# Kernel tuning notes

Hardware: AMD Instinct MI355X
Metric: run time of the kernel (lower is better)

Reference implementation:

```python
import jax, jax.numpy as jnp
import numpy as np

N_NODES = 50000
N_EDGES = 800000
IN_FEATS, HIDDEN_FEATS, NUM_CLASSES = 64, 64, 32


def setup_inputs() -> dict:
    key = jax.random.key(0)
    ks = jax.random.split(key, 9)
    features = jax.random.normal(ks[0], (N_NODES, IN_FEATS), dtype=jnp.float32)
    src = jax.random.randint(ks[1], (N_EDGES,), 0, N_NODES, dtype=jnp.int32)
    dst = jax.random.randint(ks[2], (N_EDGES,), 0, N_NODES, dtype=jnp.int32)
    def lin(k, fan_in, fan_out):
        bound = 1.0 / np.sqrt(fan_in)
        return jax.random.uniform(k, (fan_in, fan_out), jnp.float32, -bound, bound)
    W_self1 = lin(ks[3], IN_FEATS, HIDDEN_FEATS)
    W_neigh1 = lin(ks[4], IN_FEATS, HIDDEN_FEATS)
    b1 = jnp.zeros((HIDDEN_FEATS,), jnp.float32)
    W_self2 = lin(ks[5], HIDDEN_FEATS, NUM_CLASSES)
    W_neigh2 = lin(ks[6], HIDDEN_FEATS, NUM_CLASSES)
    b2 = jnp.zeros((NUM_CLASSES,), jnp.float32)
    return {"features": features, "W_self1": W_self1, "W_neigh1": W_neigh1, "b1": b1,
            "W_self2": W_self2, "W_neigh2": W_neigh2, "b2": b2, "src": src, "dst": dst}


def _sage_mean(x, W_self, W_neigh, b, src, dst, n_nodes):
    # mean over in-neighbors: edge (u, v) sends x[u] into v
    agg = jax.ops.segment_sum(x[src], dst, num_segments=n_nodes)          # [N, F]
    deg = jax.ops.segment_sum(jnp.ones((src.shape[0],), x.dtype), dst,
                              num_segments=n_nodes)                        # [N]
    h_neigh = agg / jnp.maximum(deg, 1.0)[:, None]                         # zero-in-degree -> 0
    return x @ W_self + h_neigh @ W_neigh + b


def reference(features, W_self1, W_neigh1, b1, W_self2, W_neigh2, b2, src, dst):
    n = features.shape[0]
    h = jax.nn.relu(_sage_mean(features, W_self1, W_neigh1, b1, src, dst, n))
    return _sage_mean(h, W_self2, W_neigh2, b2, src, dst, n)
```

## Files before the change

### kernel.cpp

```cpp
#include <hip/hip_runtime.h>

#define N_NODES 50000
#define N_EDGES 800000
#define NB 196
#define PBLOCKS 128
#define CHUNK 6250
#define SCAN_N (NB * PBLOCKS)
#define GEMM_BLOCKS 782

typedef unsigned short ushort_t;
typedef __attribute__((ext_vector_type(8))) short bf16x8;
typedef __attribute__((ext_vector_type(4))) float f32x4;

__device__ __forceinline__ float bflo(unsigned int u) {
    return __uint_as_float(u << 16);
}
__device__ __forceinline__ float bfhi(unsigned int u) {
    return __uint_as_float(u & 0xffff0000u);
}
__device__ __forceinline__ ushort_t f2bf(float f) {
    unsigned int x = __float_as_uint(f);
    return (ushort_t)((x + 0x7fffu + ((x >> 16) & 1u)) >> 16);
}
__device__ __forceinline__ unsigned int pack_bf(float lo, float hi) {
    return (unsigned int)f2bf(lo) | ((unsigned int)f2bf(hi) << 16);
}
__device__ __forceinline__ void split_bf(float v, short& hi, short& lo) {
    ushort_t h = f2bf(v);
    float r = v - __uint_as_float((unsigned int)h << 16);
    hi = (short)h;
    lo = (short)f2bf(r);
}


__global__ __launch_bounds__(1024)
void part_scan(const int* __restrict__ blocktot, int* __restrict__ blockstart) {
    __shared__ int psum[1024];
    constexpr int PER = (SCAN_N + 1023) / 1024;
    const int t = threadIdx.x;
    const int base = t * PER;
    int local[PER];
    int s = 0;
#pragma unroll
    for (int i = 0; i < PER; ++i) {
        int idx = base + i;
        int v = (idx < SCAN_N) ? blocktot[idx] : 0;
        local[i] = s;
        s += v;
    }
    psum[t] = s;
    __syncthreads();
    for (int off = 1; off < 1024; off <<= 1) {
        int add = (t >= off) ? psum[t - off] : 0;
        __syncthreads();
        psum[t] += add;
        __syncthreads();
    }
    const int tbase = psum[t] - s;
#pragma unroll
    for (int i = 0; i < PER; ++i) {
        int idx = base + i;
        if (idx < SCAN_N) blockstart[idx] = tbase + local[i];
    }
    if (t == 1023) blockstart[SCAN_N] = psum[1023];
}

__global__ __launch_bounds__(256)
void part_write(const int* __restrict__ src, const int* __restrict__ dst,
                const int* __restrict__ blockstart, unsigned int* __restrict__ brec) {
    __shared__ int cur[NB];
    for (int i = threadIdx.x; i < NB; i += 256)
        cur[i] = blockstart[i * PBLOCKS + blockIdx.x];
    __syncthreads();
    const int e0 = blockIdx.x * CHUNK;
    const int e1 = e0 + CHUNK;
    for (int e = e0 + (int)threadIdx.x; e < e1; e += 256) {
        int d = dst[e];
        int s = src[e];
        int pos = atomicAdd(&cur[d >> 8], 1);
        brec[pos] = ((unsigned int)(d & 255) << 16) | (unsigned int)s;
    }
}

__global__ __launch_bounds__(256)
void bucket_fill(const int* __restrict__ blockstart,
                 const unsigned int* __restrict__ brec,
                 int* __restrict__ csr_src, int* __restrict__ row_ptr) {
    __shared__ int cnt[256];
    __shared__ int cur[256];
    const int b = blockIdx.x;
    const int node0 = b * 256;
    const int w0 = blockstart[b * PBLOCKS];
    const int w1 = blockstart[(b + 1) * PBLOCKS];
    const int t = threadIdx.x;
    cnt[t] = 0;
    __syncthreads();
    for (int i = w0 + t; i < w1; i += 256)
        atomicAdd(&cnt[brec[i] >> 16], 1);
    __syncthreads();
    const int v = cnt[t];
    cur[t] = v;
    __syncthreads();
    for (int off = 1; off < 256; off <<= 1) {
        int add = (t >= off) ? cur[t - off] : 0;
        __syncthreads();
        cur[t] += add;
        __syncthreads();
    }
    const int excl = cur[t] - v;
    const int node = node0 + t;
    if (node <= N_NODES) row_ptr[node] = w0 + excl;
    __syncthreads();
    cur[t] = w0 + excl;
    __syncthreads();
    for (int i = w0 + t; i < w1; i += 256) {
        unsigned int r = brec[i];
        int pos = atomicAdd(&cur[r >> 16], 1);
        csr_src[pos] = (int)(r & 0xffffu);
    }
}

__global__ __launch_bounds__(256)
void gemm128_and_count(const float* __restrict__ A,
                       const float* __restrict__ B1,
                       const float* __restrict__ B2,
                       ushort_t* __restrict__ Cself,
                       ushort_t* __restrict__ Cn,
                       const int* __restrict__ dst,
                       int* __restrict__ blocktot) {
    __shared__ int hist[NB];

    if (blockIdx.x >= GEMM_BLOCKS) {
        const int pb = blockIdx.x - GEMM_BLOCKS;
        for (int i = threadIdx.x; i < NB; i += 256) hist[i] = 0;
        __syncthreads();
        const int e0 = pb * CHUNK;
        const int e1 = e0 + CHUNK;
        for (int e = e0 + (int)threadIdx.x; e < e1; e += 256)
            atomicAdd(&hist[dst[e] >> 8], 1);
        __syncthreads();
        for (int i = threadIdx.x; i < NB; i += 256)
            blocktot[i * PBLOCKS + pb] = hist[i];
        return;
    }

    const int l  = threadIdx.x & 63;
    const int w  = threadIdx.x >> 6;
    const int lr = l & 15;
    const int lk = (l >> 4) << 3;

    bf16x8 bhi[2][2], blo[2][2];
#pragma unroll
    for (int nt = 0; nt < 2; ++nt) {
        const int n = w * 32 + nt * 16 + lr;
        const float* Bp = (n < 64) ? (B1 + n) : (B2 + (n - 64));
#pragma unroll
        for (int ks = 0; ks < 2; ++ks) {
#pragma unroll
            for (int j = 0; j < 8; ++j) {
                float bv = Bp[(size_t)(ks * 32 + lk + j) * 64];
                short h, lo;
                split_bf(bv, h, lo);
                bhi[nt][ks][j] = h;
                blo[nt][ks][j] = lo;
            }
        }
    }

    const int m0 = blockIdx.x * 64;
    f32x4 acc[4][2];
#pragma unroll
    for (int mt = 0; mt < 4; ++mt)
#pragma unroll
        for (int nt = 0; nt < 2; ++nt) {
            f32x4 z = {0.f, 0.f, 0.f, 0.f};
            acc[mt][nt] = z;
        }

#pragma unroll
    for (int mt = 0; mt < 4; ++mt) {
        const int m = m0 + mt * 16 + lr;
        const bool valid = (m < N_NODES);
        const float* Ap = A + (size_t)m * 64 + lk;
#pragma unroll
        for (int ks = 0; ks < 2; ++ks) {
            float4 f0, f1;
            if (valid) {
                f0 = *(const float4*)(Ap + ks * 32);
                f1 = *(const float4*)(Ap + ks * 32 + 4);
            } else {
                f0 = make_float4(0.f, 0.f, 0.f, 0.f);
                f1 = f0;
            }
            const float fv[8] = {f0.x, f0.y, f0.z, f0.w, f1.x, f1.y, f1.z, f1.w};
            bf16x8 ahi, alo;
#pragma unroll
            for (int j = 0; j < 8; ++j) {
                short h, lo;
                split_bf(fv[j], h, lo);
                ahi[j] = h;
                alo[j] = lo;
            }
#pragma unroll
            for (int nt = 0; nt < 2; ++nt) {
                acc[mt][nt] = __builtin_amdgcn_mfma_f32_16x16x32_bf16(
                    ahi, bhi[nt][ks], acc[mt][nt], 0, 0, 0);
                acc[mt][nt] = __builtin_amdgcn_mfma_f32_16x16x32_bf16(
                    alo, bhi[nt][ks], acc[mt][nt], 0, 0, 0);
                acc[mt][nt] = __builtin_amdgcn_mfma_f32_16x16x32_bf16(
                    ahi, blo[nt][ks], acc[mt][nt], 0, 0, 0);
            }
        }
    }

#pragma unroll
    for (int mt = 0; mt < 4; ++mt) {
        const int mbase = m0 + mt * 16 + ((l >> 4) << 2);
#pragma unroll
        for (int nt = 0; nt < 2; ++nt) {
            const int n = w * 32 + nt * 16 + lr;
            ushort_t* T = (n < 64) ? (Cself + n) : (Cn + (n - 64));
#pragma unroll
            for (int r = 0; r < 4; ++r) {
                const int m = mbase + r;
                if (m < N_NODES) T[(size_t)m * 64] = f2bf(acc[mt][nt][r]);
            }
        }
    }
}

__global__ __launch_bounds__(256)
void gemm_cat64_bf16(const ushort_t* __restrict__ A,
                     const float* __restrict__ B1,
                     const float* __restrict__ B2,
                     ushort_t* __restrict__ Cself,
                     ushort_t* __restrict__ Cn) {
    const int l  = threadIdx.x & 63;
    const int w  = threadIdx.x >> 6;
    const int lr = l & 15;
    const int lk = (l >> 4) << 3;

    const int n = w * 16 + lr;
    const float* Bp = (n < 32) ? (B1 + n) : (B2 + (n - 32));
    bf16x8 bhi[2], blo[2];
#pragma unroll
    for (int ks = 0; ks < 2; ++ks) {
#pragma unroll
        for (int j = 0; j < 8; ++j) {
            float bv = Bp[(size_t)(ks * 32 + lk + j) * 32];
            short h, lo;
            split_bf(bv, h, lo);
            bhi[ks][j] = h;
            blo[ks][j] = lo;
        }
    }

    const int m0 = blockIdx.x * 64;
    f32x4 acc[4];
#pragma unroll
    for (int mt = 0; mt < 4; ++mt) {
        f32x4 z = {0.f, 0.f, 0.f, 0.f};
        acc[mt] = z;
    }

#pragma unroll
    for (int mt = 0; mt < 4; ++mt) {
        const int m = m0 + mt * 16 + lr;
        const bool valid = (m < N_NODES);
#pragma unroll
        for (int ks = 0; ks < 2; ++ks) {
            bf16x8 a;
            if (valid) {
                a = *(const bf16x8*)&A[(size_t)m * 64 + ks * 32 + lk];
            } else {
                bf16x8 z = {0, 0, 0, 0, 0, 0, 0, 0};
                a = z;
            }
            acc[mt] = __builtin_amdgcn_mfma_f32_16x16x32_bf16(a, bhi[ks], acc[mt], 0, 0, 0);
            acc[mt] = __builtin_amdgcn_mfma_f32_16x16x32_bf16(a, blo[ks], acc[mt], 0, 0, 0);
        }
    }

    ushort_t* T = (n < 32) ? (Cself + n) : (Cn + (n - 32));
#pragma unroll
    for (int mt = 0; mt < 4; ++mt) {
        const int mbase = m0 + mt * 16 + ((l >> 4) << 2);
#pragma unroll
        for (int r = 0; r < 4; ++r) {
            const int m = mbase + r;
            if (m < N_NODES) T[(size_t)m * 32] = f2bf(acc[mt][r]);
        }
    }
}

template <int F, bool RELU, bool OBF16>
__global__ __launch_bounds__(256)
void gather_epilogue(const ushort_t* __restrict__ Tself,
                     const ushort_t* __restrict__ Tn,
                     const int* __restrict__ row_ptr,
                     const int* __restrict__ csr_src, const float* __restrict__ bias,
                     void* __restrict__ outv) {
    constexpr int LPR = F / 8;
    constexpr int R   = 64 / LPR;
    int v = (blockIdx.x * blockDim.x + threadIdx.x) >> 6;
    int lane = threadIdx.x & 63;
    int r = lane / LPR;
    int c = lane % LPR;
    if (v >= N_NODES) return;
    int start = row_ptr[v];
    int cnt   = row_ptr[v + 1] - start;

    float a[8];
#pragma unroll
    for (int i = 0; i < 8; ++i) a[i] = 0.f;

#define ACC8(u)                                           \
    a[0] += bflo(u.x); a[1] += bfhi(u.x);                 \
    a[2] += bflo(u.y); a[3] += bfhi(u.y);                 \
    a[4] += bflo(u.z); a[5] += bfhi(u.z);                 \
    a[6] += bflo(u.w); a[7] += bfhi(u.w);

    int t = r;
    for (; t + 3 * R < cnt; t += 4 * R) {
        int s0 = csr_src[start + t];
        int s1 = csr_src[start + t + R];
        int s2 = csr_src[start + t + 2 * R];
        int s3 = csr_src[start + t + 3 * R];
        uint4 u0 = *(const uint4*)&Tn[(size_t)s0 * F + c * 8];
        uint4 u1 = *(const uint4*)&Tn[(size_t)s1 * F + c * 8];
        uint4 u2 = *(const uint4*)&Tn[(size_t)s2 * F + c * 8];
        uint4 u3 = *(const uint4*)&Tn[(size_t)s3 * F + c * 8];
        ACC8(u0) ACC8(u1) ACC8(u2) ACC8(u3)
    }
    if (t + R < cnt) {
        int s0 = csr_src[start + t];
        int s1 = csr_src[start + t + R];
        uint4 u0 = *(const uint4*)&Tn[(size_t)s0 * F + c * 8];
        uint4 u1 = *(const uint4*)&Tn[(size_t)s1 * F + c * 8];
        ACC8(u0) ACC8(u1)
        t += 2 * R;
    }
    if (t < cnt) {
        int s = csr_src[start + t];
        uint4 u = *(const uint4*)&Tn[(size_t)s * F + c * 8];
        ACC8(u)
    }
#undef ACC8

#pragma unroll
    for (int off = LPR; off < 64; off <<= 1) {
#pragma unroll
        for (int i = 0; i < 8; ++i) a[i] += __shfl_xor(a[i], off);
    }

    if (r == 0) {
        const float inv = 1.0f / (float)max(cnt, 1);
        uint4 su = *(const uint4*)&Tself[(size_t)v * F + c * 8];
        float4 bA = *(const float4*)&bias[c * 8];
        float4 bB = *(const float4*)&bias[c * 8 + 4];
        float o[8];
        o[0] = bflo(su.x) + a[0] * inv + bA.x;
        o[1] = bfhi(su.x) + a[1] * inv + bA.y;
        o[2] = bflo(su.y) + a[2] * inv + bA.z;
        o[3] = bfhi(su.y) + a[3] * inv + bA.w;
        o[4] = bflo(su.z) + a[4] * inv + bB.x;
        o[5] = bfhi(su.z) + a[5] * inv + bB.y;
        o[6] = bflo(su.w) + a[6] * inv + bB.z;
        o[7] = bfhi(su.w) + a[7] * inv + bB.w;
        if (RELU) {
#pragma unroll
            for (int i = 0; i < 8; ++i) o[i] = fmaxf(o[i], 0.f);
        }
        if (OBF16) {
            ushort_t* out = (ushort_t*)outv;
            uint4 p;
            p.x = pack_bf(o[0], o[1]); p.y = pack_bf(o[2], o[3]);
            p.z = pack_bf(o[4], o[5]); p.w = pack_bf(o[6], o[7]);
            *(uint4*)&out[(size_t)v * F + c * 8] = p;
        } else {
            float* out = (float*)outv;
            *(float4*)&out[(size_t)v * F + c * 8]     = make_float4(o[0], o[1], o[2], o[3]);
            *(float4*)&out[(size_t)v * F + c * 8 + 4] = make_float4(o[4], o[5], o[6], o[7]);
        }
    }
}

extern "C" void kernel_launch(void* const* d_in, const int* in_sizes, int n_in,
                              void* d_out, int out_size, void* d_ws, size_t ws_size,
                              hipStream_t stream) {
    const float* features = (const float*)d_in[0];
    const float* W_self1  = (const float*)d_in[1];
    const float* W_neigh1 = (const float*)d_in[2];
    const float* b1       = (const float*)d_in[3];
    const float* W_self2  = (const float*)d_in[4];
    const float* W_neigh2 = (const float*)d_in[5];
    const float* b2       = (const float*)d_in[6];
    const int*   src      = (const int*)d_in[7];
    const int*   dst      = (const int*)d_in[8];

    ushort_t* Tself1 = (ushort_t*)d_ws;
    ushort_t* Tn1    = Tself1 + (size_t)N_NODES * 64;
    ushort_t* h      = Tn1 + (size_t)N_NODES * 64;
    int* row_ptr     = (int*)(h + (size_t)N_NODES * 64);
    int* csr_src     = row_ptr + (N_NODES + 1);
    unsigned int* brec = (unsigned int*)(csr_src + N_EDGES);
    int* blocktot    = (int*)(brec + N_EDGES);
    int* blockstart  = blocktot + SCAN_N;

    ushort_t* Tself2 = Tself1;
    ushort_t* Tn2    = Tself1 + (size_t)N_NODES * 32;

    const int gather_blocks = (N_NODES + 3) / 4;

    gemm128_and_count<<<GEMM_BLOCKS + PBLOCKS, 256, 0, stream>>>(
        features, W_self1, W_neigh1, Tself1, Tn1, dst, blocktot);
    part_scan<<<1, 1024, 0, stream>>>(blocktot, blockstart);
    part_write<<<PBLOCKS, 256, 0, stream>>>(src, dst, blockstart, brec);
    bucket_fill<<<NB, 256, 0, stream>>>(blockstart, brec, csr_src, row_ptr);

    gather_epilogue<64, true, true><<<gather_blocks, 256, 0, stream>>>(
        Tself1, Tn1, row_ptr, csr_src, b1, h);

    gemm_cat64_bf16<<<GEMM_BLOCKS, 256, 0, stream>>>(h, W_self2, W_neigh2, Tself2, Tn2);

    gather_epilogue<32, false, false><<<gather_blocks, 256, 0, stream>>>(
        Tself2, Tn2, row_ptr, csr_src, b2, d_out);
}
```

Measured before the change: 185.9 us.

## Fuse layer-2 GEMM into layer-1 gather and fold partition scan into consumers

Drops the separate single-block scan kernel. part_write and bucket_fill now each recompute their partition offsets directly from the per-block histograms, and the number of partition blocks doubles. The layer-1 gather epilogue now also does the 64x64 second-layer projection per node, using register-held weight columns and wavefront shuffles. This removes the hidden-activation round trip and one GEMM launch. In exchange it adds redundant scan work in every block, 64 live weight registers per thread, and a scalar FMA projection in place of MFMA.

```diff
diff --git a/kernel.cpp b/kernel.cpp
--- a/kernel.cpp
+++ b/kernel.cpp
@@ -3,9 +3,8 @@
 #define N_NODES 50000
 #define N_EDGES 800000
 #define NB 196
-#define PBLOCKS 128
-#define CHUNK 6250
-#define SCAN_N (NB * PBLOCKS)
+#define PBLOCKS 256
+#define CHUNK 3125
 #define GEMM_BLOCKS 782
 
 typedef unsigned short ushort_t;
@@ -30,94 +29,6 @@
     float r = v - __uint_as_float((unsigned int)h << 16);
     hi = (short)h;
     lo = (short)f2bf(r);
-}
-
-
-__global__ __launch_bounds__(1024)
-void part_scan(const int* __restrict__ blocktot, int* __restrict__ blockstart) {
-    __shared__ int psum[1024];
-    constexpr int PER = (SCAN_N + 1023) / 1024;
-    const int t = threadIdx.x;
-    const int base = t * PER;
-    int local[PER];
-    int s = 0;
-#pragma unroll
-    for (int i = 0; i < PER; ++i) {
-        int idx = base + i;
-        int v = (idx < SCAN_N) ? blocktot[idx] : 0;
-        local[i] = s;
-        s += v;
-    }
-    psum[t] = s;
-    __syncthreads();
-    for (int off = 1; off < 1024; off <<= 1) {
-        int add = (t >= off) ? psum[t - off] : 0;
-        __syncthreads();
-        psum[t] += add;
-        __syncthreads();
-    }
-    const int tbase = psum[t] - s;
-#pragma unroll
-    for (int i = 0; i < PER; ++i) {
-        int idx = base + i;
-        if (idx < SCAN_N) blockstart[idx] = tbase + local[i];
-    }
-    if (t == 1023) blockstart[SCAN_N] = psum[1023];
-}
-
-__global__ __launch_bounds__(256)
-void part_write(const int* __restrict__ src, const int* __restrict__ dst,
-                const int* __restrict__ blockstart, unsigned int* __restrict__ brec) {
-    __shared__ int cur[NB];
-    for (int i = threadIdx.x; i < NB; i += 256)
-        cur[i] = blockstart[i * PBLOCKS + blockIdx.x];
-    __syncthreads();
-    const int e0 = blockIdx.x * CHUNK;
-    const int e1 = e0 + CHUNK;
-    for (int e = e0 + (int)threadIdx.x; e < e1; e += 256) {
-        int d = dst[e];
-        int s = src[e];
-        int pos = atomicAdd(&cur[d >> 8], 1);
-        brec[pos] = ((unsigned int)(d & 255) << 16) | (unsigned int)s;
-    }
-}
-
-__global__ __launch_bounds__(256)
-void bucket_fill(const int* __restrict__ blockstart,
-                 const unsigned int* __restrict__ brec,
-                 int* __restrict__ csr_src, int* __restrict__ row_ptr) {
-    __shared__ int cnt[256];
-    __shared__ int cur[256];
-    const int b = blockIdx.x;
-    const int node0 = b * 256;
-    const int w0 = blockstart[b * PBLOCKS];
-    const int w1 = blockstart[(b + 1) * PBLOCKS];
-    const int t = threadIdx.x;
-    cnt[t] = 0;
-    __syncthreads();
-    for (int i = w0 + t; i < w1; i += 256)
-        atomicAdd(&cnt[brec[i] >> 16], 1);
-    __syncthreads();
-    const int v = cnt[t];
-    cur[t] = v;
-    __syncthreads();
-    for (int off = 1; off < 256; off <<= 1) {
-        int add = (t >= off) ? cur[t - off] : 0;
-        __syncthreads();
-        cur[t] += add;
-        __syncthreads();
-    }
-    const int excl = cur[t] - v;
-    const int node = node0 + t;
-    if (node <= N_NODES) row_ptr[node] = w0 + excl;
-    __syncthreads();
-    cur[t] = w0 + excl;
-    __syncthreads();
-    for (int i = w0 + t; i < w1; i += 256) {
-        unsigned int r = brec[i];
-        int pos = atomicAdd(&cur[r >> 16], 1);
-        csr_src[pos] = (int)(r & 0xffffu);
-    }
 }
 
 __global__ __launch_bounds__(256)
@@ -230,67 +141,194 @@
 }
 
 __global__ __launch_bounds__(256)
-void gemm_cat64_bf16(const ushort_t* __restrict__ A,
-                     const float* __restrict__ B1,
-                     const float* __restrict__ B2,
-                     ushort_t* __restrict__ Cself,
-                     ushort_t* __restrict__ Cn) {
-    const int l  = threadIdx.x & 63;
-    const int w  = threadIdx.x >> 6;
-    const int lr = l & 15;
-    const int lk = (l >> 4) << 3;
-
-    const int n = w * 16 + lr;
-    const float* Bp = (n < 32) ? (B1 + n) : (B2 + (n - 32));
-    bf16x8 bhi[2], blo[2];
-#pragma unroll
-    for (int ks = 0; ks < 2; ++ks) {
-#pragma unroll
-        for (int j = 0; j < 8; ++j) {
-            float bv = Bp[(size_t)(ks * 32 + lk + j) * 32];
-            short h, lo;
-            split_bf(bv, h, lo);
-            bhi[ks][j] = h;
-            blo[ks][j] = lo;
-        }
-    }
-
-    const int m0 = blockIdx.x * 64;
-    f32x4 acc[4];
-#pragma unroll
-    for (int mt = 0; mt < 4; ++mt) {
-        f32x4 z = {0.f, 0.f, 0.f, 0.f};
-        acc[mt] = z;
-    }
-
-#pragma unroll
-    for (int mt = 0; mt < 4; ++mt) {
-        const int m = m0 + mt * 16 + lr;
-        const bool valid = (m < N_NODES);
-#pragma unroll
-        for (int ks = 0; ks < 2; ++ks) {
-            bf16x8 a;
-            if (valid) {
-                a = *(const bf16x8*)&A[(size_t)m * 64 + ks * 32 + lk];
-            } else {
-                bf16x8 z = {0, 0, 0, 0, 0, 0, 0, 0};
-                a = z;
-            }
-            acc[mt] = __builtin_amdgcn_mfma_f32_16x16x32_bf16(a, bhi[ks], acc[mt], 0, 0, 0);
-            acc[mt] = __builtin_amdgcn_mfma_f32_16x16x32_bf16(a, blo[ks], acc[mt], 0, 0, 0);
-        }
-    }
-
-    ushort_t* T = (n < 32) ? (Cself + n) : (Cn + (n - 32));
-#pragma unroll
-    for (int mt = 0; mt < 4; ++mt) {
-        const int mbase = m0 + mt * 16 + ((l >> 4) << 2);
-#pragma unroll
-        for (int r = 0; r < 4; ++r) {
-            const int m = mbase + r;
-            if (m < N_NODES) T[(size_t)m * 32] = f2bf(acc[mt][r]);
-        }
-    }
+void part_write(const int* __restrict__ src, const int* __restrict__ dst,
+                const int* __restrict__ blocktot, unsigned int* __restrict__ brec) {
+    __shared__ int ssum[256];
+    __shared__ int cur[NB];
+    const int pb = blockIdx.x;
+    const int t  = threadIdx.x;
+
+    int rsum = 0, mypart = 0;
+    if (t < NB) {
+        const int* rp = blocktot + t * PBLOCKS;
+#pragma unroll 8
+        for (int j = 0; j < PBLOCKS; ++j) {
+            if (j == pb) mypart = rsum;
+            rsum += rp[j];
+        }
+    }
+    ssum[t] = (t < NB) ? rsum : 0;
+    __syncthreads();
+    for (int off = 1; off < 256; off <<= 1) {
+        int add = (t >= off) ? ssum[t - off] : 0;
+        __syncthreads();
+        ssum[t] += add;
+        __syncthreads();
+    }
+    if (t < NB) cur[t] = (ssum[t] - rsum) + mypart;
+    __syncthreads();
+
+    const int e0 = pb * CHUNK;
+    const int e1 = e0 + CHUNK;
+    for (int e = e0 + t; e < e1; e += 256) {
+        int d = dst[e];
+        int s = src[e];
+        int pos = atomicAdd(&cur[d >> 8], 1);
+        brec[pos] = ((unsigned int)(d & 255) << 16) | (unsigned int)s;
+    }
+}
+
+__global__ __launch_bounds__(256)
+void bucket_fill(const int* __restrict__ blocktot,
+                 const unsigned int* __restrict__ brec,
+                 int* __restrict__ csr_src, int* __restrict__ row_ptr) {
+    __shared__ int ssum[256];
+    __shared__ int cnt[256];
+    __shared__ int cur[256];
+    const int b = blockIdx.x;
+    const int node0 = b * 256;
+    const int t = threadIdx.x;
+
+    int rsum = 0;
+    if (t < NB) {
+        const int* rp = blocktot + t * PBLOCKS;
+#pragma unroll 8
+        for (int j = 0; j < PBLOCKS; ++j) rsum += rp[j];
+    }
+    ssum[t] = (t < NB) ? rsum : 0;
+    __syncthreads();
+    for (int off = 1; off < 256; off <<= 1) {
+        int add = (t >= off) ? ssum[t - off] : 0;
+        __syncthreads();
+        ssum[t] += add;
+        __syncthreads();
+    }
+    const int w0 = (b == 0) ? 0 : ssum[b - 1];
+    const int w1 = ssum[b];
+    __syncthreads();
+
+    cnt[t] = 0;
+    __syncthreads();
+    for (int i = w0 + t; i < w1; i += 256)
+        atomicAdd(&cnt[brec[i] >> 16], 1);
+    __syncthreads();
+    const int v = cnt[t];
+    cur[t] = v;
+    __syncthreads();
+    for (int off = 1; off < 256; off <<= 1) {
+        int add = (t >= off) ? cur[t - off] : 0;
+        __syncthreads();
+        cur[t] += add;
+        __syncthreads();
+    }
+    const int excl = cur[t] - v;
+    const int node = node0 + t;
+    if (node <= N_NODES) row_ptr[node] = w0 + excl;
+    __syncthreads();
+    cur[t] = w0 + excl;
+    __syncthreads();
+    for (int i = w0 + t; i < w1; i += 256) {
+        unsigned int r = brec[i];
+        int pos = atomicAdd(&cur[r >> 16], 1);
+        csr_src[pos] = (int)(r & 0xffffu);
+    }
+}
+
+__global__ __launch_bounds__(256)
+void gather1_fused(const ushort_t* __restrict__ Tself,
+                   const ushort_t* __restrict__ Tn,
+                   const int* __restrict__ row_ptr,
+                   const int* __restrict__ csr_src,
+                   const float* __restrict__ bias,
+                   const float* __restrict__ Ws2,
+                   const float* __restrict__ Wn2,
+                   ushort_t* __restrict__ Tself2,
+                   ushort_t* __restrict__ Tn2) {
+    constexpr int F = 64;
+    constexpr int LPR = 8;
+    constexpr int R = 8;
+    const int lane = threadIdx.x & 63;
+
+    float wcol[64];
+    {
+        const float* Wp = (lane < 32) ? (Ws2 + lane) : (Wn2 + (lane - 32));
+#pragma unroll
+        for (int k = 0; k < 64; ++k) wcol[k] = Wp[(size_t)k * 32];
+    }
+
+    int v = (blockIdx.x * blockDim.x + threadIdx.x) >> 6;
+    if (v >= N_NODES) return;
+    const int r = lane / LPR;
+    const int c = lane % LPR;
+    int start = row_ptr[v];
+    int cnt   = row_ptr[v + 1] - start;
+
+    float a[8];
+#pragma unroll
+    for (int i = 0; i < 8; ++i) a[i] = 0.f;
+
+#define ACC8(u)                                           \
+    a[0] += bflo(u.x); a[1] += bfhi(u.x);                 \
+    a[2] += bflo(u.y); a[3] += bfhi(u.y);                 \
+    a[4] += bflo(u.z); a[5] += bfhi(u.z);                 \
+    a[6] += bflo(u.w); a[7] += bfhi(u.w);
+
+    int t = r;
+    for (; t + 3 * R < cnt; t += 4 * R) {
+        int s0 = csr_src[start + t];
+        int s1 = csr_src[start + t + R];
+        int s2 = csr_src[start + t + 2 * R];
+        int s3 = csr_src[start + t + 3 * R];
+        uint4 u0 = *(const uint4*)&Tn[(size_t)s0 * F + c * 8];
+        uint4 u1 = *(const uint4*)&Tn[(size_t)s1 * F + c * 8];
+        uint4 u2 = *(const uint4*)&Tn[(size_t)s2 * F + c * 8];
+        uint4 u3 = *(const uint4*)&Tn[(size_t)s3 * F + c * 8];
+        ACC8(u0) ACC8(u1) ACC8(u2) ACC8(u3)
+    }
+    if (t + R < cnt) {
+        int s0 = csr_src[start + t];
+        int s1 = csr_src[start + t + R];
+        uint4 u0 = *(const uint4*)&Tn[(size_t)s0 * F + c * 8];
+        uint4 u1 = *(const uint4*)&Tn[(size_t)s1 * F + c * 8];
+        ACC8(u0) ACC8(u1)
+        t += 2 * R;
+    }
+    if (t < cnt) {
+        int s = csr_src[start + t];
+        uint4 u = *(const uint4*)&Tn[(size_t)s * F + c * 8];
+        ACC8(u)
+    }
+#undef ACC8
+
+#pragma unroll
+    for (int off = LPR; off < 64; off <<= 1) {
+#pragma unroll
+        for (int i = 0; i < 8; ++i) a[i] += __shfl_xor(a[i], off);
+    }
+
+    const float inv = 1.0f / (float)max(cnt, 1);
+    uint4 su = *(const uint4*)&Tself[(size_t)v * F + c * 8];
+    float4 bA = *(const float4*)&bias[c * 8];
+    float4 bB = *(const float4*)&bias[c * 8 + 4];
+    float o[8];
+    o[0] = bflo(su.x) + a[0] * inv + bA.x;
+    o[1] = bfhi(su.x) + a[1] * inv + bA.y;
+    o[2] = bflo(su.y) + a[2] * inv + bA.z;
+    o[3] = bfhi(su.y) + a[3] * inv + bA.w;
+    o[4] = bflo(su.z) + a[4] * inv + bB.x;
+    o[5] = bfhi(su.z) + a[5] * inv + bB.y;
+    o[6] = bflo(su.w) + a[6] * inv + bB.z;
+    o[7] = bfhi(su.w) + a[7] * inv + bB.w;
+#pragma unroll
+    for (int i = 0; i < 8; ++i) o[i] = fmaxf(o[i], 0.f);
+
+    float o2 = 0.f;
+#pragma unroll
+    for (int k = 0; k < 64; ++k)
+        o2 = fmaf(__shfl(o[k & 7], k >> 3), wcol[k], o2);
+
+    if (lane < 32) Tself2[(size_t)v * 32 + lane] = f2bf(o2);
+    else           Tn2[(size_t)v * 32 + (lane - 32)] = f2bf(o2);
 }
 
 template <int F, bool RELU, bool OBF16>
@@ -400,29 +438,23 @@
 
     ushort_t* Tself1 = (ushort_t*)d_ws;
     ushort_t* Tn1    = Tself1 + (size_t)N_NODES * 64;
-    ushort_t* h      = Tn1 + (size_t)N_NODES * 64;
-    int* row_ptr     = (int*)(h + (size_t)N_NODES * 64);
+    ushort_t* T2     = Tn1 + (size_t)N_NODES * 64;
+    int* row_ptr     = (int*)(T2 + (size_t)N_NODES * 64);
     int* csr_src     = row_ptr + (N_NODES + 1);
     unsigned int* brec = (unsigned int*)(csr_src + N_EDGES);
     int* blocktot    = (int*)(brec + N_EDGES);
-    int* blockstart  = blocktot + SCAN_N;
-
-    ushort_t* Tself2 = Tself1;
-    ushort_t* Tn2    = Tself1 + (size_t)N_NODES * 32;
+
+    ushort_t* Tself2 = T2;
+    ushort_t* Tn2    = T2 + (size_t)N_NODES * 32;
 
     const int gather_blocks = (N_NODES + 3) / 4;
 
     gemm128_and_count<<<GEMM_BLOCKS + PBLOCKS, 256, 0, stream>>>(
         features, W_self1, W_neigh1, Tself1, Tn1, dst, blocktot);
-    part_scan<<<1, 1024, 0, stream>>>(blocktot, blockstart);
-    part_write<<<PBLOCKS, 256, 0, stream>>>(src, dst, blockstart, brec);
-    bucket_fill<<<NB, 256, 0, stream>>>(blockstart, brec, csr_src, row_ptr);
-
-    gather_epilogue<64, true, true><<<gather_blocks, 256, 0, stream>>>(
-        Tself1, Tn1, row_ptr, csr_src, b1, h);
-
-    gemm_cat64_bf16<<<GEMM_BLOCKS, 256, 0, stream>>>(h, W_self2, W_neigh2, Tself2, Tn2);
-
+    part_write<<<PBLOCKS, 256, 0, stream>>>(src, dst, blocktot, brec);
+    bucket_fill<<<NB, 256, 0, stream>>>(blocktot, brec, csr_src, row_ptr);
+    gather1_fused<<<gather_blocks, 256, 0, stream>>>(
+        Tself1, Tn1, row_ptr, csr_src, b1, W_self2, W_neigh2, Tself2, Tn2);
     gather_epilogue<32, false, false><<<gather_blocks, 256, 0, stream>>>(
         Tself2, Tn2, row_ptr, csr_src, b2, d_out);
 }
```

New measurement: 200.3 us. +7.8%, slower.

## Fold partition scan into write/fill kernels and gather two nodes per wave

Applied to the files above, without the earlier changes.

Removes the single-block part_scan launch. Each part_write and bucket_fill block now recomputes the bucket offsets redundantly from blocktot using row sums and a shared-memory scan. The partition block count doubles and the chunk halves. The gather kernel now handles two nodes per 64-lane wave, reading up to 32 neighbor indices cooperatively and broadcasting them with shuffles so all neighbor loads are issued at once, with a loop for the tail. This trades a serial launch and index-load latency for redundant scan work in every block and a shorter reduction.

```diff
diff --git a/kernel.cpp b/kernel.cpp
--- a/kernel.cpp
+++ b/kernel.cpp
@@ -3,9 +3,8 @@
 #define N_NODES 50000
 #define N_EDGES 800000
 #define NB 196
-#define PBLOCKS 128
-#define CHUNK 6250
-#define SCAN_N (NB * PBLOCKS)
+#define PBLOCKS 256
+#define CHUNK 3125
 #define GEMM_BLOCKS 782
 
 typedef unsigned short ushort_t;
@@ -30,94 +29,6 @@
     float r = v - __uint_as_float((unsigned int)h << 16);
     hi = (short)h;
     lo = (short)f2bf(r);
-}
-
-
-__global__ __launch_bounds__(1024)
-void part_scan(const int* __restrict__ blocktot, int* __restrict__ blockstart) {
-    __shared__ int psum[1024];
-    constexpr int PER = (SCAN_N + 1023) / 1024;
-    const int t = threadIdx.x;
-    const int base = t * PER;
-    int local[PER];
-    int s = 0;
-#pragma unroll
-    for (int i = 0; i < PER; ++i) {
-        int idx = base + i;
-        int v = (idx < SCAN_N) ? blocktot[idx] : 0;
-        local[i] = s;
-        s += v;
-    }
-    psum[t] = s;
-    __syncthreads();
-    for (int off = 1; off < 1024; off <<= 1) {
-        int add = (t >= off) ? psum[t - off] : 0;
-        __syncthreads();
-        psum[t] += add;
-        __syncthreads();
-    }
-    const int tbase = psum[t] - s;
-#pragma unroll
-    for (int i = 0; i < PER; ++i) {
-        int idx = base + i;
-        if (idx < SCAN_N) blockstart[idx] = tbase + local[i];
-    }
-    if (t == 1023) blockstart[SCAN_N] = psum[1023];
-}
-
-__global__ __launch_bounds__(256)
-void part_write(const int* __restrict__ src, const int* __restrict__ dst,
-                const int* __restrict__ blockstart, unsigned int* __restrict__ brec) {
-    __shared__ int cur[NB];
-    for (int i = threadIdx.x; i < NB; i += 256)
-        cur[i] = blockstart[i * PBLOCKS + blockIdx.x];
-    __syncthreads();
-    const int e0 = blockIdx.x * CHUNK;
-    const int e1 = e0 + CHUNK;
-    for (int e = e0 + (int)threadIdx.x; e < e1; e += 256) {
-        int d = dst[e];
-        int s = src[e];
-        int pos = atomicAdd(&cur[d >> 8], 1);
-        brec[pos] = ((unsigned int)(d & 255) << 16) | (unsigned int)s;
-    }
-}
-
-__global__ __launch_bounds__(256)
-void bucket_fill(const int* __restrict__ blockstart,
-                 const unsigned int* __restrict__ brec,
-                 int* __restrict__ csr_src, int* __restrict__ row_ptr) {
-    __shared__ int cnt[256];
-    __shared__ int cur[256];
-    const int b = blockIdx.x;
-    const int node0 = b * 256;
-    const int w0 = blockstart[b * PBLOCKS];
-    const int w1 = blockstart[(b + 1) * PBLOCKS];
-    const int t = threadIdx.x;
-    cnt[t] = 0;
-    __syncthreads();
-    for (int i = w0 + t; i < w1; i += 256)
-        atomicAdd(&cnt[brec[i] >> 16], 1);
-    __syncthreads();
-    const int v = cnt[t];
-    cur[t] = v;
-    __syncthreads();
-    for (int off = 1; off < 256; off <<= 1) {
-        int add = (t >= off) ? cur[t - off] : 0;
-        __syncthreads();
-        cur[t] += add;
-        __syncthreads();
-    }
-    const int excl = cur[t] - v;
-    const int node = node0 + t;
-    if (node <= N_NODES) row_ptr[node] = w0 + excl;
-    __syncthreads();
-    cur[t] = w0 + excl;
-    __syncthreads();
-    for (int i = w0 + t; i < w1; i += 256) {
-        unsigned int r = brec[i];
-        int pos = atomicAdd(&cur[r >> 16], 1);
-        csr_src[pos] = (int)(r & 0xffffu);
-    }
 }
 
 __global__ __launch_bounds__(256)
@@ -226,6 +137,100 @@
                 if (m < N_NODES) T[(size_t)m * 64] = f2bf(acc[mt][nt][r]);
             }
         }
+    }
+}
+
+__global__ __launch_bounds__(256)
+void part_write(const int* __restrict__ src, const int* __restrict__ dst,
+                const int* __restrict__ blocktot, unsigned int* __restrict__ brec) {
+    __shared__ int ssum[256];
+    __shared__ int cur[NB];
+    const int pb = blockIdx.x;
+    const int t  = threadIdx.x;
+
+    int rsum = 0, mypart = 0;
+    if (t < NB) {
+        const int* rp = blocktot + t * PBLOCKS;
+#pragma unroll 8
+        for (int j = 0; j < PBLOCKS; ++j) {
+            if (j == pb) mypart = rsum;
+            rsum += rp[j];
+        }
+    }
+    ssum[t] = (t < NB) ? rsum : 0;
+    __syncthreads();
+    for (int off = 1; off < 256; off <<= 1) {
+        int add = (t >= off) ? ssum[t - off] : 0;
+        __syncthreads();
+        ssum[t] += add;
+        __syncthreads();
+    }
+    if (t < NB) cur[t] = (ssum[t] - rsum) + mypart;
+    __syncthreads();
+
+    const int e0 = pb * CHUNK;
+    const int e1 = e0 + CHUNK;
+    for (int e = e0 + t; e < e1; e += 256) {
+        int d = dst[e];
+        int s = src[e];
+        int pos = atomicAdd(&cur[d >> 8], 1);
+        brec[pos] = ((unsigned int)(d & 255) << 16) | (unsigned int)s;
+    }
+}
+
+__global__ __launch_bounds__(256)
+void bucket_fill(const int* __restrict__ blocktot,
+                 const unsigned int* __restrict__ brec,
+                 int* __restrict__ csr_src, int* __restrict__ row_ptr) {
+    __shared__ int ssum[256];
+    __shared__ int cnt[256];
+    __shared__ int cur[256];
+    const int b = blockIdx.x;
+    const int node0 = b * 256;
+    const int t = threadIdx.x;
+
+    int rsum = 0;
+    if (t < NB) {
+        const int* rp = blocktot + t * PBLOCKS;
+#pragma unroll 8
+        for (int j = 0; j < PBLOCKS; ++j) rsum += rp[j];
+    }
+    ssum[t] = (t < NB) ? rsum : 0;
+    __syncthreads();
+    for (int off = 1; off < 256; off <<= 1) {
+        int add = (t >= off) ? ssum[t - off] : 0;
+        __syncthreads();
+        ssum[t] += add;
+        __syncthreads();
+    }
+    const int w0 = (b == 0) ? 0 : ssum[b - 1];
+    const int w1 = ssum[b];
+    __syncthreads();
+
+    cnt[t] = 0;
+    __syncthreads();
+    for (int i = w0 + t; i < w1; i += 256)
+        atomicAdd(&cnt[brec[i] >> 16], 1);
+    __syncthreads();
+    const int v = cnt[t];
+    cur[t] = v;
+    __syncthreads();
+    for (int off = 1; off < 256; off <<= 1) {
+        int add = (t >= off) ? cur[t - off] : 0;
+        __syncthreads();
+        cur[t] += add;
+        __syncthreads();
+    }
+    const int excl = cur[t] - v;
+    const int node = node0 + t;
+    if (node <= N_NODES) row_ptr[node] = w0 + excl;
+    __syncthreads();
+    cur[t] = w0 + excl;
+    __syncthreads();
+    for (int i = w0 + t; i < w1; i += 256) {
+        unsigned int r = brec[i];
+        int pos = atomicAdd(&cur[r >> 16], 1);
+        csr_src[pos] = (int)(r & 0xffffu);
     }
 }
 
@@ -300,15 +305,18 @@
                      const int* __restrict__ row_ptr,
                      const int* __restrict__ csr_src, const float* __restrict__ bias,
                      void* __restrict__ outv) {
-    constexpr int LPR = F / 8;
-    constexpr int R   = 64 / LPR;
-    int v = (blockIdx.x * blockDim.x + threadIdx.x) >> 6;
-    int lane = threadIdx.x & 63;
-    int r = lane / LPR;
-    int c = lane % LPR;
+    constexpr int LPR  = F / 8;
+    constexpr int G    = 32 / LPR;
+    constexpr int MAXJ = 32 / G;
+    const int lane = threadIdx.x & 63;
+    const int half = lane >> 5;
+    const int hl   = lane & 31;
+    const int r = hl / LPR;
+    const int c = hl % LPR;
+    const int v = (((int)blockIdx.x * (int)blockDim.x + (int)threadIdx.x) >> 6) * 2 + half;
     if (v >= N_NODES) return;
-    int start = row_ptr[v];
-    int cnt   = row_ptr[v + 1] - start;
+    const int start = row_ptr[v];
+    const int cnt   = row_ptr[v + 1] - start;
 
     float a[8];
 #pragma unroll
@@ -320,35 +328,36 @@
     a[4] += bflo(u.z); a[5] += bfhi(u.z);                 \
     a[6] += bflo(u.w); a[7] += bfhi(u.w);
 
-    int t = r;
-    for (; t + 3 * R < cnt; t += 4 * R) {
-        int s0 = csr_src[start + t];
-        int s1 = csr_src[start + t + R];
-        int s2 = csr_src[start + t + 2 * R];
-        int s3 = csr_src[start + t + 3 * R];
-        uint4 u0 = *(const uint4*)&Tn[(size_t)s0 * F + c * 8];
-        uint4 u1 = *(const uint4*)&Tn[(size_t)s1 * F + c * 8];
-        uint4 u2 = *(const uint4*)&Tn[(size_t)s2 * F + c * 8];
-        uint4 u3 = *(const uint4*)&Tn[(size_t)s3 * F + c * 8];
-        ACC8(u0) ACC8(u1) ACC8(u2) ACC8(u3)
-    }
-    if (t + R < cnt) {
-        int s0 = csr_src[start + t];
-        int s1 = csr_src[start + t + R];
-        uint4 u0 = *(const uint4*)&Tn[(size_t)s0 * F + c * 8];
-        uint4 u1 = *(const uint4*)&Tn[(size_t)s1 * F + c * 8];
-        ACC8(u0) ACC8(u1)
-        t += 2 * R;
-    }
-    if (t < cnt) {
-        int s = csr_src[start + t];
-        uint4 u = *(const uint4*)&Tn[(size_t)s * F + c * 8];
-        ACC8(u)
+    int idx = 0;
+    if (hl < cnt) idx = csr_src[start + hl];
+
+    const int nfast = (cnt < 32) ? cnt : 32;
+    int  sidx[MAXJ];
+    bool act[MAXJ];
+#pragma unroll
+    for (int j = 0; j < MAXJ; ++j) {
+        const int t = r + j * G;
+        act[j]  = (t < nfast);
+        sidx[j] = __shfl(idx, half * 32 + t);
+    }
+    uint4 u[MAXJ];
+#pragma unroll
+    for (int j = 0; j < MAXJ; ++j) {
+        u[j] = make_uint4(0u, 0u, 0u, 0u);
+        if (act[j]) u[j] = *(const uint4*)&Tn[(size_t)sidx[j] * F + c * 8];
+    }
+#pragma unroll
+    for (int j = 0; j < MAXJ; ++j) { ACC8(u[j]) }
+
+    for (int t = 32 + r; t < cnt; t += G) {
+        const int s = csr_src[start + t];
+        uint4 uu = *(const uint4*)&Tn[(size_t)s * F + c * 8];
+        ACC8(uu)
     }
 #undef ACC8
 
 #pragma unroll
-    for (int off = LPR; off < 64; off <<= 1) {
+    for (int off = LPR; off < 32; off <<= 1) {
 #pragma unroll
         for (int i = 0; i < 8; ++i) a[i] += __shfl_xor(a[i], off);
     }
@@ -405,24 +414,19 @@
     int* csr_src     = row_ptr + (N_NODES + 1);
     unsigned int* brec = (unsigned int*)(csr_src + N_EDGES);
     int* blocktot    = (int*)(brec + N_EDGES);
-    int* blockstart  = blocktot + SCAN_N;
 
     ushort_t* Tself2 = Tself1;
     ushort_t* Tn2    = Tself1 + (size_t)N_NODES * 32;
 
-    const int gather_blocks = (N_NODES + 3) / 4;
+    const int gather_blocks = (N_NODES + 7) / 8;
 
     gemm128_and_count<<<GEMM_BLOCKS + PBLOCKS, 256, 0, stream>>>(
         features, W_self1, W_neigh1, Tself1, Tn1, dst, blocktot);
-    part_scan<<<1, 1024, 0, stream>>>(blocktot, blockstart);
-    part_write<<<PBLOCKS, 256, 0, stream>>>(src, dst, blockstart, brec);
-    bucket_fill<<<NB, 256, 0, stream>>>(blockstart, brec, csr_src, row_ptr);
-
+    part_write<<<PBLOCKS, 256, 0, stream>>>(src, dst, blocktot, brec);
+    bucket_fill<<<NB, 256, 0, stream>>>(blocktot, brec, csr_src, row_ptr);
     gather_epilogue<64, true, true><<<gather_blocks, 256, 0, stream>>>(
         Tself1, Tn1, row_ptr, csr_src, b1, h);
-
     gemm_cat64_bf16<<<GEMM_BLOCKS, 256, 0, stream>>>(h, W_self2, W_neigh2, Tself2, Tn2);
-
     gather_epilogue<32, false, false><<<gather_blocks, 256, 0, stream>>>(
         Tself2, Tn2, row_ptr, csr_src, b2, d_out);
 }
```

Result: faster. 164.3 us (-11.6%).
